# Kernel tuning notes

Hardware: AMD Instinct MI355X
Metric: run time of the kernel (lower is better)

Reference implementation:

```python
import jax, jax.numpy as jnp
import numpy as np

NUM_HEADS = 8


def _gaussian_mha(query, key, value, gaussian, key_padding_mask,
                  in_proj_weight, in_proj_bias, out_proj_weight, out_proj_bias):
    # query: [L, N, E]; key/value: [S, N, E]; gaussian: [N*H, L, S]; key_padding_mask: [N, S] bool
    L, N, E = query.shape
    S = key.shape[0]
    H = NUM_HEADS
    Dh = E // H
    scaling = float(Dh) ** -0.5

    # split the packed in-projection (torch layout: rows are [q; k; v], y = x @ W.T + b)
    wq, wk, wv = in_proj_weight[:E], in_proj_weight[E:2 * E], in_proj_weight[2 * E:]
    bq, bk, bv = in_proj_bias[:E], in_proj_bias[E:2 * E], in_proj_bias[2 * E:]

    q = (query @ wq.T + bq) * scaling          # [L, N, E]
    k = key @ wk.T + bk                        # [S, N, E]
    v = value @ wv.T + bv                      # [S, N, E]

    # -> [N*H, L, Dh] / [N*H, S, Dh] (matches torch view+transpose)
    q = jnp.transpose(q.reshape(L, N * H, Dh), (1, 0, 2))
    k = jnp.transpose(k.reshape(S, N * H, Dh), (1, 0, 2))
    v = jnp.transpose(v.reshape(S, N * H, Dh), (1, 0, 2))

    # scores with SMCA gaussian spatial bias added pre-softmax
    scores = jnp.einsum('bld,bsd->bls', q, k) + gaussian   # [N*H, L, S]

    # key padding mask: True -> -inf, broadcast over heads and queries
    mask = key_padding_mask[:, None, None, :]              # [N, 1, 1, S]
    scores = scores.reshape(N, H, L, S)
    scores = jnp.where(mask, -jnp.inf, scores).reshape(N * H, L, S)

    attn = jax.nn.softmax(scores, axis=-1)                 # [N*H, L, S]
    out = jnp.einsum('bls,bsd->bld', attn, v)              # [N*H, L, Dh]

    # back to [L, N, E] and output projection
    out = jnp.transpose(out, (1, 0, 2)).reshape(L, N, E)
    return out @ out_proj_weight.T + out_proj_bias


def setup_inputs() -> dict:
    key = jax.random.key(0)
    ks = jax.random.split(key, 8)
    L, S, N, E, H = 300, 1024, 32, 256, NUM_HEADS
    return {
        'query': jax.random.normal(ks[0], (L, N, E), jnp.float32),
        'key': jax.random.normal(ks[1], (S, N, E), jnp.float32),
        'value': jax.random.normal(ks[2], (S, N, E), jnp.float32),
        'gaussian': jax.random.normal(ks[3], (N * H, L, S), jnp.float32),
        'key_padding_mask': jnp.zeros((N, S), jnp.bool_),
        'in_proj_weight': jax.random.normal(ks[4], (3 * E, E), jnp.float32) * (E ** -0.5),
        'in_proj_bias': jax.random.normal(ks[5], (3 * E,), jnp.float32) * 0.02,
        'out_proj_weight': jax.random.normal(ks[6], (E, E), jnp.float32) * (E ** -0.5),
        'out_proj_bias': jax.random.normal(ks[7], (E,), jnp.float32) * 0.02,
    }


def reference(query, key, value, gaussian, key_padding_mask,
              in_proj_weight, in_proj_bias, out_proj_weight, out_proj_bias):
    return _gaussian_mha(query, key, value, gaussian, key_padding_mask,
                         in_proj_weight, in_proj_bias, out_proj_weight, out_proj_bias)
```

## Files before the change

### kernel.cpp

```cpp
#include <hip/hip_runtime.h>

#define LQ 300
#define NB 32
#define SK 1024
#define EE 256
#define HH 8
#define DH 32
#define BH 256
#define LPAD 304
#define NLT 19

typedef short short8 __attribute__((ext_vector_type(8)));
typedef short short4v __attribute__((ext_vector_type(4)));
typedef float f32x4 __attribute__((ext_vector_type(4)));

#define MFMA16(a, b, c) __builtin_amdgcn_mfma_f32_16x16x32_bf16((a), (b), (c), 0, 0, 0)

__device__ __forceinline__ short f2bf(float f) {
    unsigned u = __float_as_uint(f);
    u += 0x7FFFu + ((u >> 16) & 1u);
    return (short)(u >> 16);
}

__device__ __forceinline__ short8 cvt8(const float* __restrict__ p) {
    float4 x = *(const float4*)p;
    float4 y = *(const float4*)(p + 4);
    short8 r;
    r[0] = f2bf(x.x); r[1] = f2bf(x.y); r[2] = f2bf(x.z); r[3] = f2bf(x.w);
    r[4] = f2bf(y.x); r[5] = f2bf(y.y); r[6] = f2bf(y.z); r[7] = f2bf(y.w);
    return r;
}

__global__ __launch_bounds__(256) void prep_kernel(
    const float* __restrict__ ipw, const float* __restrict__ opw,
    short* __restrict__ wbf)
{
    int i = blockIdx.x * 256 + threadIdx.x;
    int base = i * 4;
    const float* src = (base < 3 * EE * EE) ? (ipw + base) : (opw + base - 3 * EE * EE);
    float4 x = *(const float4*)src;
    short4v r;
    r[0] = f2bf(x.x); r[1] = f2bf(x.y); r[2] = f2bf(x.z); r[3] = f2bf(x.w);
    *(short4v*)(wbf + base) = r;
}

__global__ __launch_bounds__(256) void proj_kernel(
    const float* __restrict__ query, const float* __restrict__ key,
    const float* __restrict__ value, const short* __restrict__ wbf,
    const float* __restrict__ bias,
    short* __restrict__ qws, short* __restrict__ kws, short* __restrict__ vws)
{
    int wave = (blockIdx.x * 256 + threadIdx.x) >> 6;
    int lid = threadIdx.x & 63, quad = lid >> 4, l16 = lid & 15;

    int u = wave, p;
    const float* X;
    if (u < 600)             { p = 0; X = query; }
    else if (u < 600 + 2048) { p = 1; X = key;   u -= 600; }
    else                     { p = 2; X = value; u -= 2648; }
    int t = u * 16 + l16;

    const short* wb = wbf + p * EE * EE;
    f32x4 acc[16];
    #pragma unroll
    for (int f = 0; f < 16; f++) acc[f] = (f32x4){0.f, 0.f, 0.f, 0.f};

    for (int ks = 0; ks < 8; ks++) {
        short8 af = cvt8(X + (size_t)t * EE + ks * 32 + quad * 8);
        #pragma unroll
        for (int f = 0; f < 16; f++) {
            short8 bf = *(const short8*)(wb + (size_t)(f * 16 + l16) * EE + ks * 32 + quad * 8);
            acc[f] = MFMA16(af, bf, acc[f]);
        }
    }

    int tokbase = (wave < 600 ? wave : u) * 16;
    #pragma unroll
    for (int f = 0; f < 16; f++) {
        int feat = f * 16 + l16;
        float bia = bias[p * EE + feat];
        int h = feat >> 5, d = feat & 31;
        #pragma unroll
        for (int r = 0; r < 4; r++) {
            int tok = tokbase + quad * 4 + r;
            float v = acc[f][r] + bia;
            int n = tok & 31, s = tok >> 5;
            int b = n * HH + h;
            if (p == 0) {
                v *= 0.17677669529663687f;
                qws[((size_t)b * LPAD + s) * DH + d] = f2bf(v);
            } else if (p == 1) {
                kws[((size_t)b * SK + s) * DH + d] = f2bf(v);
            } else {
                vws[((size_t)b * SK + s) * DH + d] = f2bf(v);
            }
        }
    }
}

__global__ __launch_bounds__(256) void vtrans_kernel(
    const short* __restrict__ vws, short* __restrict__ vt)
{
    __shared__ __align__(16) short tile[32][272];
    int b = blockIdx.x >> 2, s0 = (blockIdx.x & 3) * 256;
    const short* src = vws + ((size_t)b * SK + s0) * DH;
    #pragma unroll
    for (int pass = 0; pass < 4; pass++) {
        int i = pass * 256 + threadIdx.x;
        int sl = i >> 2, d0 = (i & 3) * 8;
        short8 x = *(const short8*)(src + sl * DH + d0);
        #pragma unroll
        for (int j = 0; j < 8; j++) tile[d0 + j][sl] = x[j];
    }
    __syncthreads();
    short* dst = vt + (size_t)b * DH * SK + s0;
    #pragma unroll
    for (int pass = 0; pass < 4; pass++) {
        int i = pass * 256 + threadIdx.x;
        int d = i >> 5, sl0 = (i & 31) * 8;
        *(short8*)(dst + (size_t)d * SK + sl0) = *(const short8*)(&tile[d][sl0]);
    }
}

__global__ __launch_bounds__(256) void attn_kernel(
    const short* __restrict__ qws, const short* __restrict__ kws,
    const short* __restrict__ vt, const float* __restrict__ gauss,
    const unsigned char* __restrict__ mask, short* __restrict__ ows)
{
    __shared__ __align__(16) float smem[4][16 * 64];
    __shared__ float mbuf[4][16];
    __shared__ float lbuf[4][16];

    int bid = blockIdx.x;
    int swzb = (bid & 7) * ((BH * NLT) >> 3) + (bid >> 3);
    int b = swzb / NLT, lt = swzb % NLT;

    int wv = threadIdx.x >> 6;
    int lid = threadIdx.x & 63, quad = lid >> 4, l16 = lid & 15;
    int n = b >> 3, h = b & 7;

    int ql = lt * 16 + l16;
    short8 qa = *(const short8*)(qws + ((size_t)b * LPAD + ql) * DH + quad * 8);

    f32x4 o0 = {0.f, 0.f, 0.f, 0.f}, o1 = {0.f, 0.f, 0.f, 0.f};
    float mr = -3e38f, ls = 0.f;

    const float* gbase = gauss + (size_t)b * LQ * SK;
    const float* grow[4];
    #pragma unroll
    for (int r = 0; r < 4; r++) {
        int l = lt * 16 + quad * 4 + r;
        grow[r] = gbase + (size_t)(l < LQ ? l : LQ - 1) * SK + l16;
    }

    float* sl = smem[wv];
    int sbase = wv * 256;

    int rk = l16 & 7;
    int ra0 = l16 * 64 + (((quad * 2 + 0) ^ rk) << 2);
    int ra1 = l16 * 64 + (((quad * 2 + 1) ^ rk) << 2);
    int ra2 = l16 * 64 + (((quad * 2 + 8) ^ rk) << 2);
    int ra3 = l16 * 64 + (((quad * 2 + 9) ^ rk) << 2);

    for (int it = 0; it < 4; it++) {
        int sc = sbase + it * 64;

        short8 kb[4];
        #pragma unroll
        for (int c = 0; c < 4; c++)
            kb[c] = *(const short8*)(kws + ((size_t)b * SK + sc + c * 16 + l16) * DH + quad * 8);

        short8 vb[2][2];
        #pragma unroll
        for (int t2 = 0; t2 < 2; t2++)
            #pragma unroll
            for (int k2 = 0; k2 < 2; k2++)
                vb[t2][k2] = *(const short8*)(vt + ((size_t)b * DH + t2 * 16 + l16) * SK + sc + k2 * 32 + quad * 8);

        bool mk[4];
        #pragma unroll
        for (int c = 0; c < 4; c++) mk[c] = mask[n * SK + sc + c * 16 + l16] != 0;

        float g[4][4];
        #pragma unroll
        for (int r = 0; r < 4; r++)
            #pragma unroll
            for (int c = 0; c < 4; c++) g[r][c] = grow[r][sc + c * 16];

        f32x4 z = {0.f, 0.f, 0.f, 0.f};
        f32x4 cc[4];
        #pragma unroll
        for (int c = 0; c < 4; c++) cc[c] = MFMA16(qa, kb[c], z);

        #pragma unroll
        for (int r = 0; r < 4; r++) {
            int row = quad * 4 + r;
            int rowoff = row * 64;
            int rkw = row & 7;
            #pragma unroll
            for (int c = 0; c < 4; c++) {
                float s = mk[c] ? -3e38f : (cc[c][r] + g[r][c]);
                int colg = c * 4 + (l16 >> 2);
                sl[rowoff + (((colg ^ rkw) << 2) + (l16 & 3))] = s;
            }
        }

        asm volatile("s_waitcnt lgkmcnt(0)" ::: "memory");

        f32x4 s0 = *(const f32x4*)(sl + ra0);
        f32x4 s1 = *(const f32x4*)(sl + ra1);
        f32x4 s2 = *(const f32x4*)(sl + ra2);
        f32x4 s3 = *(const f32x4*)(sl + ra3);

        float mxa = fmaxf(fmaxf(fmaxf(s0[0], s0[1]), fmaxf(s0[2], s0[3])),
                          fmaxf(fmaxf(s1[0], s1[1]), fmaxf(s1[2], s1[3])));
        float mxb = fmaxf(fmaxf(fmaxf(s2[0], s2[1]), fmaxf(s2[2], s2[3])),
                          fmaxf(fmaxf(s3[0], s3[1]), fmaxf(s3[2], s3[3])));
        float mx = fmaxf(mxa, mxb);
        mx = fmaxf(mx, __shfl_xor(mx, 16, 64));
        mx = fmaxf(mx, __shfl_xor(mx, 32, 64));

        float nm = fmaxf(mr, mx);
        float al = __expf(mr - nm);

        float p[16];
        #pragma unroll
        for (int j = 0; j < 4; j++) {
            p[j]      = __expf(s0[j] - nm);
            p[4 + j]  = __expf(s1[j] - nm);
            p[8 + j]  = __expf(s2[j] - nm);
            p[12 + j] = __expf(s3[j] - nm);
        }
        float sm = 0.f;
        #pragma unroll
        for (int j = 0; j < 16; j++) sm += p[j];
        sm += __shfl_xor(sm, 16, 64);
        sm += __shfl_xor(sm, 32, 64);

        ls = ls * al + sm;
        mr = nm;

        int albits = __float_as_int(al);
        #pragma unroll
        for (int r = 0; r < 4; r++) {
            float alr = __int_as_float(
                __builtin_amdgcn_ds_bpermute(4 * (quad * 4 + r), albits));
            o0[r] *= alr;
            o1[r] *= alr;
        }

        short8 pa0, pa1;
        #pragma unroll
        for (int j = 0; j < 4; j++) {
            pa0[j]     = f2bf(p[j]);
            pa0[4 + j] = f2bf(p[4 + j]);
            pa1[j]     = f2bf(p[8 + j]);
            pa1[4 + j] = f2bf(p[12 + j]);
        }

        o0 = MFMA16(pa0, vb[0][0], o0);
        o0 = MFMA16(pa1, vb[0][1], o0);
        o1 = MFMA16(pa0, vb[1][0], o1);
        o1 = MFMA16(pa1, vb[1][1], o1);
    }

    asm volatile("s_waitcnt lgkmcnt(0)" ::: "memory");
    #pragma unroll
    for (int r = 0; r < 4; r++) {
        int row = quad * 4 + r;
        sl[row * 32 + l16]      = o0[r];
        sl[row * 32 + 16 + l16] = o1[r];
    }
    if (quad == 0) { mbuf[wv][l16] = mr; lbuf[wv][l16] = ls; }
    __syncthreads();

    int row = threadIdx.x >> 4, col = threadIdx.x & 15;
    float M = -3e38f;
    #pragma unroll
    for (int w = 0; w < 4; w++) M = fmaxf(M, mbuf[w][row]);
    float L = 0.f, a0 = 0.f, a1 = 0.f;
    #pragma unroll
    for (int w = 0; w < 4; w++) {
        float e = __expf(mbuf[w][row] - M);
        L += e * lbuf[w][row];
        a0 += e * smem[w][row * 32 + col];
        a1 += e * smem[w][row * 32 + 16 + col];
    }
    int l = lt * 16 + row;
    if (l < LQ) {
        float inv = 1.0f / L;
        size_t base = ((size_t)l * NB + n) * EE + h * DH;
        ows[base + col]      = f2bf(a0 * inv);
        ows[base + 16 + col] = f2bf(a1 * inv);
    }
}

__global__ __launch_bounds__(256) void oproj_kernel(
    const short* __restrict__ xa, const short* __restrict__ wbf,
    const float* __restrict__ bias, float* __restrict__ out)
{
    int wave = (blockIdx.x * 256 + threadIdx.x) >> 6;
    int lid = threadIdx.x & 63, quad = lid >> 4, l16 = lid & 15;
    int t = wave * 16 + l16;

    const short* wb = wbf + 3 * EE * EE;
    f32x4 acc[16];
    #pragma unroll
    for (int f = 0; f < 16; f++) acc[f] = (f32x4){0.f, 0.f, 0.f, 0.f};

    for (int ks = 0; ks < 8; ks++) {
        short8 af = *(const short8*)(xa + (size_t)t * EE + ks * 32 + quad * 8);
        #pragma unroll
        for (int f = 0; f < 16; f++) {
            short8 bf = *(const short8*)(wb + (size_t)(f * 16 + l16) * EE + ks * 32 + quad * 8);
            acc[f] = MFMA16(af, bf, acc[f]);
        }
    }

    #pragma unroll
    for (int f = 0; f < 16; f++) {
        int e = f * 16 + l16;
        float bi = bias[e];
        #pragma unroll
        for (int r = 0; r < 4; r++) {
            int tok = wave * 16 + quad * 4 + r;
            out[(size_t)tok * EE + e] = acc[f][r] + bi;
        }
    }
}

extern "C" void kernel_launch(void* const* d_in, const int* in_sizes, int n_in,
                              void* d_out, int out_size, void* d_ws, size_t ws_size,
                              hipStream_t stream) {
    const float* query = (const float*)d_in[0];
    const float* key   = (const float*)d_in[1];
    const float* value = (const float*)d_in[2];
    const float* gauss = (const float*)d_in[3];
    const unsigned char* mask = (const unsigned char*)d_in[4];
    const float* ipw = (const float*)d_in[5];
    const float* ipb = (const float*)d_in[6];
    const float* opw = (const float*)d_in[7];
    const float* opb = (const float*)d_in[8];
    float* out = (float*)d_out;

    short* wbf = (short*)d_ws;
    short* qws = wbf + 4 * EE * EE;
    short* kws = qws + (size_t)BH * LPAD * DH;
    short* vws = kws + (size_t)BH * SK * DH;
    short* vt  = vws + (size_t)BH * SK * DH;
    short* ows = vt  + (size_t)BH * SK * DH;

    prep_kernel<<<256, 256, 0, stream>>>(ipw, opw, wbf);
    proj_kernel<<<1174, 256, 0, stream>>>(query, key, value, wbf, ipb, qws, kws, vws);
    vtrans_kernel<<<1024, 256, 0, stream>>>(vws, vt);
    attn_kernel<<<BH * NLT, 256, 0, stream>>>(qws, kws, vt, gauss, mask, ows);
    oproj_kernel<<<150, 256, 0, stream>>>(ows, wbf, opb, out);
}
```

Before: 592.0 us.

## Assign each wave its own query rows over full key range; lazy rescale

Before, the four waves of a block split the key range for one 16-row query tile and merged their partial softmax results through shared memory. Now each wave owns a distinct 16-row query tile and walks all 1024 keys, so the block covers 64 query rows and the cross-wave merge and __syncthreads are gone. The gaussian bias and mask are loaded as vectors in the post-transpose layout, which gives contiguous float4 reads instead of scalar strided loads. Online-softmax rescaling is skipped unless the running max grows by more than a threshold (8). The trade-off is far fewer blocks, each looping longer, and some padded rows wasted in the last tile.

```diff
diff --git a/kernel.cpp b/kernel.cpp
--- a/kernel.cpp
+++ b/kernel.cpp
@@ -8,7 +8,7 @@
 #define DH 32
 #define BH 256
 #define LPAD 304
-#define NLT 19
+#define NLB 5
 
 typedef short short8 __attribute__((ext_vector_type(8)));
 typedef short short4v __attribute__((ext_vector_type(4)));
@@ -128,42 +128,35 @@
     const unsigned char* __restrict__ mask, short* __restrict__ ows)
 {
     __shared__ __align__(16) float smem[4][16 * 64];
-    __shared__ float mbuf[4][16];
-    __shared__ float lbuf[4][16];
 
     int bid = blockIdx.x;
-    int swzb = (bid & 7) * ((BH * NLT) >> 3) + (bid >> 3);
-    int b = swzb / NLT, lt = swzb % NLT;
+    int swzb = (bid & 7) * ((BH * NLB) >> 3) + (bid >> 3);
+    int b = swzb / NLB, lt = swzb % NLB;
 
     int wv = threadIdx.x >> 6;
     int lid = threadIdx.x & 63, quad = lid >> 4, l16 = lid & 15;
     int n = b >> 3, h = b & 7;
 
-    int ql = lt * 16 + l16;
-    short8 qa = *(const short8*)(qws + ((size_t)b * LPAD + ql) * DH + quad * 8);
+    int l0 = lt * 64 + wv * 16;
+    int qrow = l0 + l16; if (qrow > LPAD - 1) qrow = LPAD - 1;
+    short8 qa = *(const short8*)(qws + ((size_t)b * LPAD + qrow) * DH + quad * 8);
+
+    int grow = l0 + l16; if (grow > LQ - 1) grow = LQ - 1;
+    const float* gl = gauss + ((size_t)b * LQ + grow) * SK;
+    const unsigned char* mrow = mask + (size_t)n * SK;
 
     f32x4 o0 = {0.f, 0.f, 0.f, 0.f}, o1 = {0.f, 0.f, 0.f, 0.f};
     float mr = -3e38f, ls = 0.f;
 
-    const float* gbase = gauss + (size_t)b * LQ * SK;
-    const float* grow[4];
-    #pragma unroll
-    for (int r = 0; r < 4; r++) {
-        int l = lt * 16 + quad * 4 + r;
-        grow[r] = gbase + (size_t)(l < LQ ? l : LQ - 1) * SK + l16;
-    }
-
     float* sl = smem[wv];
-    int sbase = wv * 256;
-
     int rk = l16 & 7;
     int ra0 = l16 * 64 + (((quad * 2 + 0) ^ rk) << 2);
     int ra1 = l16 * 64 + (((quad * 2 + 1) ^ rk) << 2);
     int ra2 = l16 * 64 + (((quad * 2 + 8) ^ rk) << 2);
     int ra3 = l16 * 64 + (((quad * 2 + 9) ^ rk) << 2);
 
-    for (int it = 0; it < 4; it++) {
-        int sc = sbase + it * 64;
+    for (int it = 0; it < 16; it++) {
+        int sc = it * 64;
 
         short8 kb[4];
         #pragma unroll
@@ -177,15 +170,15 @@
             for (int k2 = 0; k2 < 2; k2++)
                 vb[t2][k2] = *(const short8*)(vt + ((size_t)b * DH + t2 * 16 + l16) * SK + sc + k2 * 32 + quad * 8);
 
-        bool mk[4];
-        #pragma unroll
-        for (int c = 0; c < 4; c++) mk[c] = mask[n * SK + sc + c * 16 + l16] != 0;
-
-        float g[4][4];
-        #pragma unroll
-        for (int r = 0; r < 4; r++)
-            #pragma unroll
-            for (int c = 0; c < 4; c++) g[r][c] = grow[r][sc + c * 16];
+        f32x4 g0 = *(const f32x4*)(gl + sc + quad * 8);
+        f32x4 g1 = *(const f32x4*)(gl + sc + quad * 8 + 4);
+        f32x4 g2 = *(const f32x4*)(gl + sc + 32 + quad * 8);
+        f32x4 g3 = *(const f32x4*)(gl + sc + 32 + quad * 8 + 4);
+
+        const unsigned* mp0 = (const unsigned*)(mrow + sc + quad * 8);
+        unsigned mk0 = mp0[0], mk1 = mp0[1];
+        const unsigned* mp1 = (const unsigned*)(mrow + sc + 32 + quad * 8);
+        unsigned mk2 = mp1[0], mk3 = mp1[1];
 
         f32x4 z = {0.f, 0.f, 0.f, 0.f};
         f32x4 cc[4];
@@ -199,9 +192,8 @@
             int rkw = row & 7;
             #pragma unroll
             for (int c = 0; c < 4; c++) {
-                float s = mk[c] ? -3e38f : (cc[c][r] + g[r][c]);
                 int colg = c * 4 + (l16 >> 2);
-                sl[rowoff + (((colg ^ rkw) << 2) + (l16 & 3))] = s;
+                sl[rowoff + (((colg ^ rkw) << 2) + (l16 & 3))] = cc[c][r];
             }
         }
 
@@ -211,6 +203,14 @@
         f32x4 s1 = *(const f32x4*)(sl + ra1);
         f32x4 s2 = *(const f32x4*)(sl + ra2);
         f32x4 s3 = *(const f32x4*)(sl + ra3);
+
+        #pragma unroll
+        for (int j = 0; j < 4; j++) {
+            s0[j] = ((mk0 >> (8 * j)) & 0xffu) ? -3e38f : (s0[j] + g0[j]);
+            s1[j] = ((mk1 >> (8 * j)) & 0xffu) ? -3e38f : (s1[j] + g1[j]);
+            s2[j] = ((mk2 >> (8 * j)) & 0xffu) ? -3e38f : (s2[j] + g2[j]);
+            s3[j] = ((mk3 >> (8 * j)) & 0xffu) ? -3e38f : (s3[j] + g3[j]);
+        }
 
         float mxa = fmaxf(fmaxf(fmaxf(s0[0], s0[1]), fmaxf(s0[2], s0[3])),
                           fmaxf(fmaxf(s1[0], s1[1]), fmaxf(s1[2], s1[3])));
@@ -220,34 +220,35 @@
         mx = fmaxf(mx, __shfl_xor(mx, 16, 64));
         mx = fmaxf(mx, __shfl_xor(mx, 32, 64));
 
-        float nm = fmaxf(mr, mx);
-        float al = __expf(mr - nm);
+        if (!__all(mx <= mr + 8.f)) {
+            float nm = fmaxf(mr, mx);
+            float al = __expf(mr - nm);
+            mr = nm;
+            ls *= al;
+            int albits = __float_as_int(al);
+            #pragma unroll
+            for (int r = 0; r < 4; r++) {
+                float alr = __int_as_float(
+                    __builtin_amdgcn_ds_bpermute(4 * (quad * 4 + r), albits));
+                o0[r] *= alr;
+                o1[r] *= alr;
+            }
+        }
 
         float p[16];
         #pragma unroll
         for (int j = 0; j < 4; j++) {
-            p[j]      = __expf(s0[j] - nm);
-            p[4 + j]  = __expf(s1[j] - nm);
-            p[8 + j]  = __expf(s2[j] - nm);
-            p[12 + j] = __expf(s3[j] - nm);
+            p[j]      = __expf(s0[j] - mr);
+            p[4 + j]  = __expf(s1[j] - mr);
+            p[8 + j]  = __expf(s2[j] - mr);
+            p[12 + j] = __expf(s3[j] - mr);
         }
         float sm = 0.f;
         #pragma unroll
         for (int j = 0; j < 16; j++) sm += p[j];
         sm += __shfl_xor(sm, 16, 64);
         sm += __shfl_xor(sm, 32, 64);
-
-        ls = ls * al + sm;
-        mr = nm;
-
-        int albits = __float_as_int(al);
-        #pragma unroll
-        for (int r = 0; r < 4; r++) {
-            float alr = __int_as_float(
-                __builtin_amdgcn_ds_bpermute(4 * (quad * 4 + r), albits));
-            o0[r] *= alr;
-            o1[r] *= alr;
-        }
+        ls += sm;
 
         short8 pa0, pa1;
         #pragma unroll
@@ -264,34 +265,18 @@
         o1 = MFMA16(pa1, vb[1][1], o1);
     }
 
-    asm volatile("s_waitcnt lgkmcnt(0)" ::: "memory");
+    float inv = 1.0f / ls;
+    int invbits = __float_as_int(inv);
     #pragma unroll
     for (int r = 0; r < 4; r++) {
-        int row = quad * 4 + r;
-        sl[row * 32 + l16]      = o0[r];
-        sl[row * 32 + 16 + l16] = o1[r];
-    }
-    if (quad == 0) { mbuf[wv][l16] = mr; lbuf[wv][l16] = ls; }
-    __syncthreads();
-
-    int row = threadIdx.x >> 4, col = threadIdx.x & 15;
-    float M = -3e38f;
-    #pragma unroll
-    for (int w = 0; w < 4; w++) M = fmaxf(M, mbuf[w][row]);
-    float L = 0.f, a0 = 0.f, a1 = 0.f;
-    #pragma unroll
-    for (int w = 0; w < 4; w++) {
-        float e = __expf(mbuf[w][row] - M);
-        L += e * lbuf[w][row];
-        a0 += e * smem[w][row * 32 + col];
-        a1 += e * smem[w][row * 32 + 16 + col];
-    }
-    int l = lt * 16 + row;
-    if (l < LQ) {
-        float inv = 1.0f / L;
-        size_t base = ((size_t)l * NB + n) * EE + h * DH;
-        ows[base + col]      = f2bf(a0 * inv);
-        ows[base + 16 + col] = f2bf(a1 * inv);
+        float invr = __int_as_float(
+            __builtin_amdgcn_ds_bpermute(4 * (quad * 4 + r), invbits));
+        int l = l0 + quad * 4 + r;
+        if (l < LQ) {
+            size_t base = ((size_t)l * NB + n) * EE + h * DH;
+            ows[base + l16]      = f2bf(o0[r] * invr);
+            ows[base + 16 + l16] = f2bf(o1[r] * invr);
+        }
     }
 }
 
@@ -353,6 +338,6 @@
     prep_kernel<<<256, 256, 0, stream>>>(ipw, opw, wbf);
     proj_kernel<<<1174, 256, 0, stream>>>(query, key, value, wbf, ipb, qws, kws, vws);
     vtrans_kernel<<<1024, 256, 0, stream>>>(vws, vt);
-    attn_kernel<<<BH * NLT, 256, 0, stream>>>(qws, kws, vt, gauss, mask, ows);
+    attn_kernel<<<BH * NLB, 256, 0, stream>>>(qws, kws, vt, gauss, mask, ows);
     oproj_kernel<<<150, 256, 0, stream>>>(ows, wbf, opb, out);
 }
```

Measured after the change: 612.3 us. 1.03x slower.

## Vectorize gaussian/mask loads in softmax layout, prefetch next tile, lazy rescale

Applied to the files above, without the earlier changes.

The gaussian bias and padding mask are now loaded as contiguous float4 and packed-byte vectors, laid out to match the post-LDS softmax layout, and added after the LDS transpose instead of before it. This replaces strided scalar loads with wide coalesced ones. The next tile's gaussian and mask are prefetched one iteration ahead using register double-buffering, and the loop is fully unrolled. The online-softmax rescale is skipped whenever the new max exceeds the running max by at most 8. This saves exp and bpermute work but lets probabilities reach about e^8 before bf16 conversion, and it uses more registers.

```diff
diff --git a/kernel.cpp b/kernel.cpp
--- a/kernel.cpp
+++ b/kernel.cpp
@@ -142,16 +142,12 @@
     int ql = lt * 16 + l16;
     short8 qa = *(const short8*)(qws + ((size_t)b * LPAD + ql) * DH + quad * 8);
 
+    int grow = lt * 16 + l16; if (grow > LQ - 1) grow = LQ - 1;
+    const float* gl = gauss + ((size_t)b * LQ + grow) * SK;
+    const unsigned char* mrow = mask + (size_t)n * SK;
+
     f32x4 o0 = {0.f, 0.f, 0.f, 0.f}, o1 = {0.f, 0.f, 0.f, 0.f};
     float mr = -3e38f, ls = 0.f;
-
-    const float* gbase = gauss + (size_t)b * LQ * SK;
-    const float* grow[4];
-    #pragma unroll
-    for (int r = 0; r < 4; r++) {
-        int l = lt * 16 + quad * 4 + r;
-        grow[r] = gbase + (size_t)(l < LQ ? l : LQ - 1) * SK + l16;
-    }
 
     float* sl = smem[wv];
     int sbase = wv * 256;
@@ -162,6 +158,16 @@
     int ra2 = l16 * 64 + (((quad * 2 + 8) ^ rk) << 2);
     int ra3 = l16 * 64 + (((quad * 2 + 9) ^ rk) << 2);
 
+    f32x4 g0 = *(const f32x4*)(gl + sbase + quad * 8);
+    f32x4 g1 = *(const f32x4*)(gl + sbase + quad * 8 + 4);
+    f32x4 g2 = *(const f32x4*)(gl + sbase + 32 + quad * 8);
+    f32x4 g3 = *(const f32x4*)(gl + sbase + 32 + quad * 8 + 4);
+    unsigned mk0 = ((const unsigned*)(mrow + sbase + quad * 8))[0];
+    unsigned mk1 = ((const unsigned*)(mrow + sbase + quad * 8))[1];
+    unsigned mk2 = ((const unsigned*)(mrow + sbase + 32 + quad * 8))[0];
+    unsigned mk3 = ((const unsigned*)(mrow + sbase + 32 + quad * 8))[1];
+
+    #pragma unroll
     for (int it = 0; it < 4; it++) {
         int sc = sbase + it * 64;
 
@@ -176,16 +182,6 @@
             #pragma unroll
             for (int k2 = 0; k2 < 2; k2++)
                 vb[t2][k2] = *(const short8*)(vt + ((size_t)b * DH + t2 * 16 + l16) * SK + sc + k2 * 32 + quad * 8);
-
-        bool mk[4];
-        #pragma unroll
-        for (int c = 0; c < 4; c++) mk[c] = mask[n * SK + sc + c * 16 + l16] != 0;
-
-        float g[4][4];
-        #pragma unroll
-        for (int r = 0; r < 4; r++)
-            #pragma unroll
-            for (int c = 0; c < 4; c++) g[r][c] = grow[r][sc + c * 16];
 
         f32x4 z = {0.f, 0.f, 0.f, 0.f};
         f32x4 cc[4];
@@ -199,9 +195,8 @@
             int rkw = row & 7;
             #pragma unroll
             for (int c = 0; c < 4; c++) {
-                float s = mk[c] ? -3e38f : (cc[c][r] + g[r][c]);
                 int colg = c * 4 + (l16 >> 2);
-                sl[rowoff + (((colg ^ rkw) << 2) + (l16 & 3))] = s;
+                sl[rowoff + (((colg ^ rkw) << 2) + (l16 & 3))] = cc[c][r];
             }
         }
 
@@ -211,6 +206,25 @@
         f32x4 s1 = *(const f32x4*)(sl + ra1);
         f32x4 s2 = *(const f32x4*)(sl + ra2);
         f32x4 s3 = *(const f32x4*)(sl + ra3);
+
+        int itn = (it + 1) & 3;
+        int scn = sbase + itn * 64;
+        f32x4 h0 = *(const f32x4*)(gl + scn + quad * 8);
+        f32x4 h1 = *(const f32x4*)(gl + scn + quad * 8 + 4);
+        f32x4 h2 = *(const f32x4*)(gl + scn + 32 + quad * 8);
+        f32x4 h3 = *(const f32x4*)(gl + scn + 32 + quad * 8 + 4);
+        unsigned nk0 = ((const unsigned*)(mrow + scn + quad * 8))[0];
+        unsigned nk1 = ((const unsigned*)(mrow + scn + quad * 8))[1];
+        unsigned nk2 = ((const unsigned*)(mrow + scn + 32 + quad * 8))[0];
+        unsigned nk3 = ((const unsigned*)(mrow + scn + 32 + quad * 8))[1];
+
+        #pragma unroll
+        for (int j = 0; j < 4; j++) {
+            s0[j] = ((mk0 >> (8 * j)) & 0xffu) ? -3e38f : (s0[j] + g0[j]);
+            s1[j] = ((mk1 >> (8 * j)) & 0xffu) ? -3e38f : (s1[j] + g1[j]);
+            s2[j] = ((mk2 >> (8 * j)) & 0xffu) ? -3e38f : (s2[j] + g2[j]);
+            s3[j] = ((mk3 >> (8 * j)) & 0xffu) ? -3e38f : (s3[j] + g3[j]);
+        }
 
         float mxa = fmaxf(fmaxf(fmaxf(s0[0], s0[1]), fmaxf(s0[2], s0[3])),
                           fmaxf(fmaxf(s1[0], s1[1]), fmaxf(s1[2], s1[3])));
@@ -220,34 +234,35 @@
         mx = fmaxf(mx, __shfl_xor(mx, 16, 64));
         mx = fmaxf(mx, __shfl_xor(mx, 32, 64));
 
-        float nm = fmaxf(mr, mx);
-        float al = __expf(mr - nm);
+        if (!__all(mx <= mr + 8.f)) {
+            float nm = fmaxf(mr, mx);
+            float al = __expf(mr - nm);
+            mr = nm;
+            ls *= al;
+            int albits = __float_as_int(al);
+            #pragma unroll
+            for (int r = 0; r < 4; r++) {
+                float alr = __int_as_float(
+                    __builtin_amdgcn_ds_bpermute(4 * (quad * 4 + r), albits));
+                o0[r] *= alr;
+                o1[r] *= alr;
+            }
+        }
 
         float p[16];
         #pragma unroll
         for (int j = 0; j < 4; j++) {
-            p[j]      = __expf(s0[j] - nm);
-            p[4 + j]  = __expf(s1[j] - nm);
-            p[8 + j]  = __expf(s2[j] - nm);
-            p[12 + j] = __expf(s3[j] - nm);
+            p[j]      = __expf(s0[j] - mr);
+            p[4 + j]  = __expf(s1[j] - mr);
+            p[8 + j]  = __expf(s2[j] - mr);
+            p[12 + j] = __expf(s3[j] - mr);
         }
         float sm = 0.f;
         #pragma unroll
         for (int j = 0; j < 16; j++) sm += p[j];
         sm += __shfl_xor(sm, 16, 64);
         sm += __shfl_xor(sm, 32, 64);
-
-        ls = ls * al + sm;
-        mr = nm;
-
-        int albits = __float_as_int(al);
-        #pragma unroll
-        for (int r = 0; r < 4; r++) {
-            float alr = __int_as_float(
-                __builtin_amdgcn_ds_bpermute(4 * (quad * 4 + r), albits));
-            o0[r] *= alr;
-            o1[r] *= alr;
-        }
+        ls += sm;
 
         short8 pa0, pa1;
         #pragma unroll
@@ -262,6 +277,9 @@
         o0 = MFMA16(pa1, vb[0][1], o0);
         o1 = MFMA16(pa0, vb[1][0], o1);
         o1 = MFMA16(pa1, vb[1][1], o1);
+
+        g0 = h0; g1 = h1; g2 = h2; g3 = h3;
+        mk0 = nk0; mk1 = nk1; mk2 = nk2; mk3 = nk3;
     }
 
     asm volatile("s_waitcnt lgkmcnt(0)" ::: "memory");
```

After: 593.4 us. About the same (+0.2%).
